# Kernel tuning notes

Hardware: AMD Instinct MI355X
Metric: run time of the kernel (lower is better)

Reference implementation:

```python
import jax, jax.numpy as jnp
import numpy as np

B = 524288       # number of parallel tracklets
S_DIM = 8        # state dim [x,y,z,vx,vy,vz,ax,ay]
O_DIM = 3        # observation dim [x,y,z]
DT = 0.1         # delta_t in seconds (10 Hz tracker step)


def build_F(dt: float) -> jnp.ndarray:
    """Constant-acceleration transition matrix, [8,8]."""
    dt2 = 0.5 * dt * dt
    F = np.eye(S_DIM, dtype=np.float32)
    F[0, 3] = dt; F[1, 4] = dt; F[2, 5] = dt
    F[0, 6] = dt2; F[1, 7] = dt2
    F[3, 6] = dt; F[4, 7] = dt
    return jnp.asarray(F)


def setup_inputs() -> dict:
    key = jax.random.key(0)
    kx, kP, kz = jax.random.split(key, 3)
    x = jax.random.normal(kx, (B, S_DIM, 1), dtype=jnp.float32)
    # PSD covariance: I + 0.1 * L @ L^T  (well-conditioned, non-trivial)
    L = 0.1 * jax.random.normal(kP, (B, S_DIM, S_DIM), dtype=jnp.float32)
    P = jnp.broadcast_to(jnp.eye(S_DIM, dtype=jnp.float32), (B, S_DIM, S_DIM)) \
        + jnp.matmul(L, jnp.swapaxes(L, -1, -2))
    z = jax.random.normal(kz, (B, O_DIM, 1), dtype=jnp.float32)
    # default process / measurement noise, as in the module's registered buffers
    Q = jnp.broadcast_to(0.01 * jnp.eye(S_DIM, dtype=jnp.float32), (B, S_DIM, S_DIM))
    R = jnp.broadcast_to(0.10 * jnp.eye(O_DIM, dtype=jnp.float32), (B, O_DIM, O_DIM))
    return {"x": x, "P": P, "z": z, "Q": Q, "R": R}


def reference(x, P, z, Q, R):
    """Batched EKF predict(DT, Q) followed by update(z, R).

    H = [I_3 | 0] selects the first 3 state components, so H @ A and A @ H^T
    are implemented as row/column slices (identical math, no materialized H).
    """
    F = build_F(DT)  # [8,8]
    # --- predict ---
    x_pred = jnp.einsum('ij,bjk->bik', F, x)             # [B,8,1]
    P_pred = jnp.einsum('ij,bjk,lk->bil', F, P, F) + Q   # F P F^T + Q, [B,8,8]
    # --- update ---
    S = P_pred[:, :O_DIM, :O_DIM] + R                    # H P H^T + R, [B,3,3]
    K = jnp.matmul(P_pred[:, :, :O_DIM], jnp.linalg.inv(S))  # P H^T S^{-1}, [B,8,3]
    innov = z - x_pred[:, :O_DIM, :]                     # z - H x, [B,3,1]
    x_upd = x_pred + jnp.matmul(K, innov)                # [B,8,1]
    # (I - K H) P = P - K (H P) = P - K @ P_pred[:, :3, :]
    P_upd = P_pred - jnp.matmul(K, P_pred[:, :O_DIM, :])  # [B,8,8]
    return x_upd, P_upd
```

## Files before the change

kernel.cpp:

```cpp
#include <hip/hip_runtime.h>


#define DT_C  0.1f
#define DT2_C 0.005f

__global__ __launch_bounds__(256) void ekf_kernel(
    const float* __restrict__ x_in,
    const float* __restrict__ P_in,
    const float* __restrict__ z_in,
    const float* __restrict__ Q_in,
    const float* __restrict__ R_in,
    float* __restrict__ out_x,
    float* __restrict__ out_P,
    int B)
{
    int b = blockIdx.x * blockDim.x + threadIdx.x;
    if (b >= B) return;

    float x[8];
    {
        const float4* p = reinterpret_cast<const float4*>(x_in + (size_t)b * 8);
        float4 a0 = p[0], a1 = p[1];
        x[0]=a0.x; x[1]=a0.y; x[2]=a0.z; x[3]=a0.w;
        x[4]=a1.x; x[5]=a1.y; x[6]=a1.z; x[7]=a1.w;
    }

    float P[64];
    {
        const float4* p = reinterpret_cast<const float4*>(P_in + (size_t)b * 64);
        #pragma unroll
        for (int i = 0; i < 16; ++i) {
            float4 v = p[i];
            P[4*i+0]=v.x; P[4*i+1]=v.y; P[4*i+2]=v.z; P[4*i+3]=v.w;
        }
    }

    float xp[8];
    xp[0] = x[0] + DT_C*x[3] + DT2_C*x[6];
    xp[1] = x[1] + DT_C*x[4] + DT2_C*x[7];
    xp[2] = x[2] + DT_C*x[5];
    xp[3] = x[3] + DT_C*x[6];
    xp[4] = x[4] + DT_C*x[7];
    xp[5] = x[5];
    xp[6] = x[6];
    xp[7] = x[7];

    #pragma unroll
    for (int j = 0; j < 8; ++j) {
        P[0*8+j] += DT_C*P[3*8+j] + DT2_C*P[6*8+j];
        P[1*8+j] += DT_C*P[4*8+j] + DT2_C*P[7*8+j];
        P[2*8+j] += DT_C*P[5*8+j];
        P[3*8+j] += DT_C*P[6*8+j];
        P[4*8+j] += DT_C*P[7*8+j];
    }
    #pragma unroll
    for (int i = 0; i < 8; ++i) {
        P[i*8+0] += DT_C*P[i*8+3] + DT2_C*P[i*8+6];
        P[i*8+1] += DT_C*P[i*8+4] + DT2_C*P[i*8+7];
        P[i*8+2] += DT_C*P[i*8+5];
        P[i*8+3] += DT_C*P[i*8+6];
        P[i*8+4] += DT_C*P[i*8+7];
    }
    {
        const float4* p = reinterpret_cast<const float4*>(Q_in + (size_t)b * 64);
        #pragma unroll
        for (int i = 0; i < 16; ++i) {
            float4 v = p[i];
            P[4*i+0]+=v.x; P[4*i+1]+=v.y; P[4*i+2]+=v.z; P[4*i+3]+=v.w;
        }
    }

    const float* Rb = R_in + (size_t)b * 9;
    float sa = P[0]  + Rb[0], sb = P[1]  + Rb[1], sc = P[2]  + Rb[2];
    float sd = P[8]  + Rb[3], se = P[9]  + Rb[4], sf = P[10] + Rb[5];
    float sg = P[16] + Rb[6], sh = P[17] + Rb[7], si = P[18] + Rb[8];

    float A0 = se*si - sf*sh;
    float A1 = sf*sg - sd*si;
    float A2 = sd*sh - se*sg;
    float det = sa*A0 + sb*A1 + sc*A2;
    float idet = 1.0f / det;
    float i00 = A0*idet;
    float i01 = (sc*sh - sb*si)*idet;
    float i02 = (sb*sf - sc*se)*idet;
    float i10 = A1*idet;
    float i11 = (sa*si - sc*sg)*idet;
    float i12 = (sc*sd - sa*sf)*idet;
    float i20 = A2*idet;
    float i21 = (sb*sg - sa*sh)*idet;
    float i22 = (sa*se - sb*sd)*idet;

    float K0[8], K1[8], K2[8];
    #pragma unroll
    for (int i = 0; i < 8; ++i) {
        float p0 = P[i*8+0], p1 = P[i*8+1], p2 = P[i*8+2];
        K0[i] = p0*i00 + p1*i10 + p2*i20;
        K1[i] = p0*i01 + p1*i11 + p2*i21;
        K2[i] = p0*i02 + p1*i12 + p2*i22;
    }

    const float* zb = z_in + (size_t)b * 3;
    float v0 = zb[0] - xp[0];
    float v1 = zb[1] - xp[1];
    float v2 = zb[2] - xp[2];

    {
        float xu[8];
        #pragma unroll
        for (int i = 0; i < 8; ++i)
            xu[i] = xp[i] + K0[i]*v0 + K1[i]*v1 + K2[i]*v2;
        float4* oxp = reinterpret_cast<float4*>(out_x + (size_t)b * 8);
        oxp[0] = make_float4(xu[0],xu[1],xu[2],xu[3]);
        oxp[1] = make_float4(xu[4],xu[5],xu[6],xu[7]);
    }

    float T0[8], T1[8], T2[8];
    #pragma unroll
    for (int j = 0; j < 8; ++j) { T0[j]=P[j]; T1[j]=P[8+j]; T2[j]=P[16+j]; }

    float4* oPp = reinterpret_cast<float4*>(out_P + (size_t)b * 64);
    #pragma unroll
    for (int i = 0; i < 8; ++i) {
        float r[8];
        #pragma unroll
        for (int j = 0; j < 8; ++j)
            r[j] = P[i*8+j] - (K0[i]*T0[j] + K1[i]*T1[j] + K2[i]*T2[j]);
        oPp[2*i+0] = make_float4(r[0],r[1],r[2],r[3]);
        oPp[2*i+1] = make_float4(r[4],r[5],r[6],r[7]);
    }
}

extern "C" void kernel_launch(void* const* d_in, const int* in_sizes, int n_in,
                              void* d_out, int out_size, void* d_ws, size_t ws_size,
                              hipStream_t stream) {
    const float* x = (const float*)d_in[0];
    const float* P = (const float*)d_in[1];
    const float* z = (const float*)d_in[2];
    const float* Q = (const float*)d_in[3];
    const float* R = (const float*)d_in[4];
    int B = in_sizes[0] / 8;

    float* out   = (float*)d_out;
    float* out_x = out;
    float* out_P = out + (size_t)B * 8;

    int block = 256;
    int grid = (B + block - 1) / block;
    ekf_kernel<<<grid, block, 0, stream>>>(x, P, z, Q, R, out_x, out_P, B);
}
```

Measured before the change: 399.5 us.

## Stage P, Q and R through LDS for coalesced global loads and stores

Each 64-thread block cooperatively loads its P, Q and R tiles from global memory with consecutive threads reading consecutive float4s. The tiles go into padded LDS, and each thread then reads its own matrix from there. Results are written back to LDS and stored out coalesced. A separate tail kernel handles leftover elements. This targets the strided per-thread 256-byte access pattern, at the cost of LDS usage, two barriers and reduced occupancy from the large shared allocation.

```diff
diff --git a/kernel.cpp b/kernel.cpp
--- a/kernel.cpp
+++ b/kernel.cpp
@@ -4,47 +4,10 @@
 #define DT_C  0.1f
 #define DT2_C 0.005f
 
-__global__ __launch_bounds__(256) void ekf_kernel(
-    const float* __restrict__ x_in,
-    const float* __restrict__ P_in,
-    const float* __restrict__ z_in,
-    const float* __restrict__ Q_in,
-    const float* __restrict__ R_in,
-    float* __restrict__ out_x,
-    float* __restrict__ out_P,
-    int B)
-{
-    int b = blockIdx.x * blockDim.x + threadIdx.x;
-    if (b >= B) return;
-
-    float x[8];
-    {
-        const float4* p = reinterpret_cast<const float4*>(x_in + (size_t)b * 8);
-        float4 a0 = p[0], a1 = p[1];
-        x[0]=a0.x; x[1]=a0.y; x[2]=a0.z; x[3]=a0.w;
-        x[4]=a1.x; x[5]=a1.y; x[6]=a1.z; x[7]=a1.w;
-    }
-
-    float P[64];
-    {
-        const float4* p = reinterpret_cast<const float4*>(P_in + (size_t)b * 64);
-        #pragma unroll
-        for (int i = 0; i < 16; ++i) {
-            float4 v = p[i];
-            P[4*i+0]=v.x; P[4*i+1]=v.y; P[4*i+2]=v.z; P[4*i+3]=v.w;
-        }
-    }
-
-    float xp[8];
-    xp[0] = x[0] + DT_C*x[3] + DT2_C*x[6];
-    xp[1] = x[1] + DT_C*x[4] + DT2_C*x[7];
-    xp[2] = x[2] + DT_C*x[5];
-    xp[3] = x[3] + DT_C*x[6];
-    xp[4] = x[4] + DT_C*x[7];
-    xp[5] = x[5];
-    xp[6] = x[6];
-    xp[7] = x[7];
-
+#define TPB   64
+#define ROWV4 17
+
+__device__ __forceinline__ void ekf_predict_rows_cols(float* P) {
     #pragma unroll
     for (int j = 0; j < 8; ++j) {
         P[0*8+j] += DT_C*P[3*8+j] + DT2_C*P[6*8+j];
@@ -61,19 +24,14 @@
         P[i*8+3] += DT_C*P[i*8+6];
         P[i*8+4] += DT_C*P[i*8+7];
     }
-    {
-        const float4* p = reinterpret_cast<const float4*>(Q_in + (size_t)b * 64);
-        #pragma unroll
-        for (int i = 0; i < 16; ++i) {
-            float4 v = p[i];
-            P[4*i+0]+=v.x; P[4*i+1]+=v.y; P[4*i+2]+=v.z; P[4*i+3]+=v.w;
-        }
-    }
-
-    const float* Rb = R_in + (size_t)b * 9;
-    float sa = P[0]  + Rb[0], sb = P[1]  + Rb[1], sc = P[2]  + Rb[2];
-    float sd = P[8]  + Rb[3], se = P[9]  + Rb[4], sf = P[10] + Rb[5];
-    float sg = P[16] + Rb[6], sh = P[17] + Rb[7], si = P[18] + Rb[8];
+}
+
+__device__ __forceinline__ void ekf_update(float* P, const float* xp,
+                                           float z0, float z1, float z2,
+                                           const float* Rl, float* xu) {
+    float sa = P[0]  + Rl[0], sb = P[1]  + Rl[1], sc = P[2]  + Rl[2];
+    float sd = P[8]  + Rl[3], se = P[9]  + Rl[4], sf = P[10] + Rl[5];
+    float sg = P[16] + Rl[6], sh = P[17] + Rl[7], si = P[18] + Rl[8];
 
     float A0 = se*si - sf*sh;
     float A1 = sf*sg - sd*si;
@@ -99,35 +57,187 @@
         K2[i] = p0*i02 + p1*i12 + p2*i22;
     }
 
-    const float* zb = z_in + (size_t)b * 3;
-    float v0 = zb[0] - xp[0];
-    float v1 = zb[1] - xp[1];
-    float v2 = zb[2] - xp[2];
-
-    {
-        float xu[8];
+    float v0 = z0 - xp[0];
+    float v1 = z1 - xp[1];
+    float v2 = z2 - xp[2];
+
+    #pragma unroll
+    for (int i = 0; i < 8; ++i)
+        xu[i] = xp[i] + K0[i]*v0 + K1[i]*v1 + K2[i]*v2;
+
+    float T0[8], T1[8], T2[8];
+    #pragma unroll
+    for (int j = 0; j < 8; ++j) { T0[j]=P[j]; T1[j]=P[8+j]; T2[j]=P[16+j]; }
+    #pragma unroll
+    for (int i = 0; i < 8; ++i) {
         #pragma unroll
-        for (int i = 0; i < 8; ++i)
-            xu[i] = xp[i] + K0[i]*v0 + K1[i]*v1 + K2[i]*v2;
-        float4* oxp = reinterpret_cast<float4*>(out_x + (size_t)b * 8);
+        for (int j = 0; j < 8; ++j)
+            P[i*8+j] -= K0[i]*T0[j] + K1[i]*T1[j] + K2[i]*T2[j];
+    }
+}
+
+__global__ __launch_bounds__(TPB) void ekf_kernel(
+    const float* __restrict__ x_in,
+    const float* __restrict__ P_in,
+    const float* __restrict__ z_in,
+    const float* __restrict__ Q_in,
+    const float* __restrict__ R_in,
+    float* __restrict__ out_x,
+    float* __restrict__ out_P)
+{
+    __shared__ float4 ldsP[TPB * ROWV4];
+    __shared__ float4 ldsQ[TPB * ROWV4];
+    __shared__ float  ldsR[TPB * 9];
+
+    const int t = threadIdx.x;
+    const long long blockBase = (long long)blockIdx.x * TPB;
+    const long long b = blockBase + t;
+
+    const float4* Pg = reinterpret_cast<const float4*>(P_in) + blockBase * 16;
+    const float4* Qg = reinterpret_cast<const float4*>(Q_in) + blockBase * 16;
+    const float*  Rg = R_in + blockBase * 9;
+
+    #pragma unroll
+    for (int k = 0; k < 16; ++k) {
+        int i = k * TPB + t;
+        int e = i >> 4, c = i & 15;
+        ldsP[e * ROWV4 + c] = Pg[i];
+        ldsQ[e * ROWV4 + c] = Qg[i];
+    }
+    #pragma unroll
+    for (int k = 0; k < 9; ++k) {
+        int i = k * TPB + t;
+        ldsR[i] = Rg[i];
+    }
+
+    float x[8];
+    {
+        const float4* p = reinterpret_cast<const float4*>(x_in + b * 8);
+        float4 a0 = p[0], a1 = p[1];
+        x[0]=a0.x; x[1]=a0.y; x[2]=a0.z; x[3]=a0.w;
+        x[4]=a1.x; x[5]=a1.y; x[6]=a1.z; x[7]=a1.w;
+    }
+    const float* zb = z_in + b * 3;
+    float z0 = zb[0], z1 = zb[1], z2 = zb[2];
+
+    __syncthreads();
+
+    float P[64];
+    #pragma unroll
+    for (int j = 0; j < 16; ++j) {
+        float4 v = ldsP[t * ROWV4 + j];
+        P[4*j+0]=v.x; P[4*j+1]=v.y; P[4*j+2]=v.z; P[4*j+3]=v.w;
+    }
+
+    float xp[8];
+    xp[0] = x[0] + DT_C*x[3] + DT2_C*x[6];
+    xp[1] = x[1] + DT_C*x[4] + DT2_C*x[7];
+    xp[2] = x[2] + DT_C*x[5];
+    xp[3] = x[3] + DT_C*x[6];
+    xp[4] = x[4] + DT_C*x[7];
+    xp[5] = x[5];
+    xp[6] = x[6];
+    xp[7] = x[7];
+
+    ekf_predict_rows_cols(P);
+
+    #pragma unroll
+    for (int j = 0; j < 16; ++j) {
+        float4 v = ldsQ[t * ROWV4 + j];
+        P[4*j+0]+=v.x; P[4*j+1]+=v.y; P[4*j+2]+=v.z; P[4*j+3]+=v.w;
+    }
+
+    float Rl[9];
+    #pragma unroll
+    for (int j = 0; j < 9; ++j) Rl[j] = ldsR[t * 9 + j];
+
+    float xu[8];
+    ekf_update(P, xp, z0, z1, z2, Rl, xu);
+
+    {
+        float4* oxp = reinterpret_cast<float4*>(out_x + b * 8);
         oxp[0] = make_float4(xu[0],xu[1],xu[2],xu[3]);
         oxp[1] = make_float4(xu[4],xu[5],xu[6],xu[7]);
     }
 
-    float T0[8], T1[8], T2[8];
-    #pragma unroll
-    for (int j = 0; j < 8; ++j) { T0[j]=P[j]; T1[j]=P[8+j]; T2[j]=P[16+j]; }
+    #pragma unroll
+    for (int j = 0; j < 16; ++j)
+        ldsP[t * ROWV4 + j] = make_float4(P[4*j+0],P[4*j+1],P[4*j+2],P[4*j+3]);
+
+    __syncthreads();
+
+    float4* Pog = reinterpret_cast<float4*>(out_P) + blockBase * 16;
+    #pragma unroll
+    for (int k = 0; k < 16; ++k) {
+        int i = k * TPB + t;
+        Pog[i] = ldsP[(i >> 4) * ROWV4 + (i & 15)];
+    }
+}
+
+__global__ __launch_bounds__(TPB) void ekf_tail_kernel(
+    const float* __restrict__ x_in,
+    const float* __restrict__ P_in,
+    const float* __restrict__ z_in,
+    const float* __restrict__ Q_in,
+    const float* __restrict__ R_in,
+    float* __restrict__ out_x,
+    float* __restrict__ out_P,
+    int first, int B)
+{
+    int b = first + (int)threadIdx.x;
+    if (b >= B) return;
+
+    float x[8];
+    {
+        const float4* p = reinterpret_cast<const float4*>(x_in + (size_t)b * 8);
+        float4 a0 = p[0], a1 = p[1];
+        x[0]=a0.x; x[1]=a0.y; x[2]=a0.z; x[3]=a0.w;
+        x[4]=a1.x; x[5]=a1.y; x[6]=a1.z; x[7]=a1.w;
+    }
+    float P[64];
+    {
+        const float4* p = reinterpret_cast<const float4*>(P_in + (size_t)b * 64);
+        #pragma unroll
+        for (int i = 0; i < 16; ++i) {
+            float4 v = p[i];
+            P[4*i+0]=v.x; P[4*i+1]=v.y; P[4*i+2]=v.z; P[4*i+3]=v.w;
+        }
+    }
+    float xp[8];
+    xp[0] = x[0] + DT_C*x[3] + DT2_C*x[6];
+    xp[1] = x[1] + DT_C*x[4] + DT2_C*x[7];
+    xp[2] = x[2] + DT_C*x[5];
+    xp[3] = x[3] + DT_C*x[6];
+    xp[4] = x[4] + DT_C*x[7];
+    xp[5] = x[5]; xp[6] = x[6]; xp[7] = x[7];
+
+    ekf_predict_rows_cols(P);
+
+    {
+        const float4* p = reinterpret_cast<const float4*>(Q_in + (size_t)b * 64);
+        #pragma unroll
+        for (int i = 0; i < 16; ++i) {
+            float4 v = p[i];
+            P[4*i+0]+=v.x; P[4*i+1]+=v.y; P[4*i+2]+=v.z; P[4*i+3]+=v.w;
+        }
+    }
+    const float* Rb = R_in + (size_t)b * 9;
+    float Rl[9];
+    #pragma unroll
+    for (int j = 0; j < 9; ++j) Rl[j] = Rb[j];
+    const float* zb = z_in + (size_t)b * 3;
+
+    float xu[8];
+    ekf_update(P, xp, zb[0], zb[1], zb[2], Rl, xu);
+
+    float4* oxp = reinterpret_cast<float4*>(out_x + (size_t)b * 8);
+    oxp[0] = make_float4(xu[0],xu[1],xu[2],xu[3]);
+    oxp[1] = make_float4(xu[4],xu[5],xu[6],xu[7]);
 
     float4* oPp = reinterpret_cast<float4*>(out_P + (size_t)b * 64);
     #pragma unroll
-    for (int i = 0; i < 8; ++i) {
-        float r[8];
-        #pragma unroll
-        for (int j = 0; j < 8; ++j)
-            r[j] = P[i*8+j] - (K0[i]*T0[j] + K1[i]*T1[j] + K2[i]*T2[j]);
-        oPp[2*i+0] = make_float4(r[0],r[1],r[2],r[3]);
-        oPp[2*i+1] = make_float4(r[4],r[5],r[6],r[7]);
-    }
+    for (int i = 0; i < 16; ++i)
+        oPp[i] = make_float4(P[4*i+0],P[4*i+1],P[4*i+2],P[4*i+3]);
 }
 
 extern "C" void kernel_launch(void* const* d_in, const int* in_sizes, int n_in,
@@ -144,7 +254,11 @@
     float* out_x = out;
     float* out_P = out + (size_t)B * 8;
 
-    int block = 256;
-    int grid = (B + block - 1) / block;
-    ekf_kernel<<<grid, block, 0, stream>>>(x, P, z, Q, R, out_x, out_P, B);
-}
+    int fullBlocks = B / TPB;
+    int rem = B % TPB;
+    if (fullBlocks > 0)
+        ekf_kernel<<<fullBlocks, TPB, 0, stream>>>(x, P, z, Q, R, out_x, out_P);
+    if (rem > 0)
+        ekf_tail_kernel<<<1, TPB, 0, stream>>>(x, P, z, Q, R, out_x, out_P,
+                                               fullBlocks * TPB, B);
+}
```

Measured after the change: 356.6 us. -10.7%, faster.

## Split each tracklet across 8 lanes, one covariance row per lane, using shuffles

Applied to the files above, without the earlier changes.

Instead of one thread holding the full 8x8 covariance, eight lanes each hold one row and exchange data through width-8 shuffles for the row update of F P F^T, the S matrix, and the K H P correction. Neighbouring lanes now read adjacent rows, so loads and stores coalesce better, and register pressure drops enough that a min-blocks-per-SM launch bound is added. The price is extra shuffle instructions and a 3x3 inverse that every lane of the group computes redundantly.

```diff
diff --git a/kernel.cpp b/kernel.cpp
--- a/kernel.cpp
+++ b/kernel.cpp
@@ -4,7 +4,7 @@
 #define DT_C  0.1f
 #define DT2_C 0.005f
 
-__global__ __launch_bounds__(256) void ekf_kernel(
+__global__ __launch_bounds__(256, 4) void ekf_kernel(
     const float* __restrict__ x_in,
     const float* __restrict__ P_in,
     const float* __restrict__ z_in,
@@ -14,66 +14,56 @@
     float* __restrict__ out_P,
     int B)
 {
-    int b = blockIdx.x * blockDim.x + threadIdx.x;
-    if (b >= B) return;
+    const long long tid = (long long)blockIdx.x * blockDim.x + threadIdx.x;
+    const long long e = tid >> 3;
+    const int r = (int)(tid & 7);
+    if (e >= B) return;
 
-    float x[8];
+    float p[8];
     {
-        const float4* p = reinterpret_cast<const float4*>(x_in + (size_t)b * 8);
-        float4 a0 = p[0], a1 = p[1];
-        x[0]=a0.x; x[1]=a0.y; x[2]=a0.z; x[3]=a0.w;
-        x[4]=a1.x; x[5]=a1.y; x[6]=a1.z; x[7]=a1.w;
+        const float4* Pg = reinterpret_cast<const float4*>(P_in + e * 64 + r * 8);
+        float4 a = Pg[0], b = Pg[1];
+        p[0]=a.x; p[1]=a.y; p[2]=a.z; p[3]=a.w;
+        p[4]=b.x; p[5]=b.y; p[6]=b.z; p[7]=b.w;
+    }
+    float xr = x_in[e * 8 + r];
+
+    const float coefA = (r <= 4) ? DT_C  : 0.0f;
+    const float coefB = (r <= 1) ? DT2_C : 0.0f;
+    const int srcA = (r + 3) & 7;
+    const int srcB = (r + 6) & 7;
+
+    float pn[8];
+    #pragma unroll
+    for (int j = 0; j < 8; ++j) {
+        float vA = __shfl(p[j], srcA, 8);
+        float vB = __shfl(p[j], srcB, 8);
+        pn[j] = p[j] + coefA * vA + coefB * vB;
     }
 
-    float P[64];
+    float xp = xr + coefA * __shfl(xr, srcA, 8) + coefB * __shfl(xr, srcB, 8);
+
+    pn[0] += DT_C*pn[3] + DT2_C*pn[6];
+    pn[1] += DT_C*pn[4] + DT2_C*pn[7];
+    pn[2] += DT_C*pn[5];
+    pn[3] += DT_C*pn[6];
+    pn[4] += DT_C*pn[7];
+
     {
-        const float4* p = reinterpret_cast<const float4*>(P_in + (size_t)b * 64);
-        #pragma unroll
-        for (int i = 0; i < 16; ++i) {
-            float4 v = p[i];
-            P[4*i+0]=v.x; P[4*i+1]=v.y; P[4*i+2]=v.z; P[4*i+3]=v.w;
-        }
+        const float4* Qg = reinterpret_cast<const float4*>(Q_in + e * 64 + r * 8);
+        float4 a = Qg[0], b = Qg[1];
+        pn[0]+=a.x; pn[1]+=a.y; pn[2]+=a.z; pn[3]+=a.w;
+        pn[4]+=b.x; pn[5]+=b.y; pn[6]+=b.z; pn[7]+=b.w;
     }
 
-    float xp[8];
-    xp[0] = x[0] + DT_C*x[3] + DT2_C*x[6];
-    xp[1] = x[1] + DT_C*x[4] + DT2_C*x[7];
-    xp[2] = x[2] + DT_C*x[5];
-    xp[3] = x[3] + DT_C*x[6];
-    xp[4] = x[4] + DT_C*x[7];
-    xp[5] = x[5];
-    xp[6] = x[6];
-    xp[7] = x[7];
+    float t00 = __shfl(pn[0], 0, 8), t01 = __shfl(pn[1], 0, 8), t02 = __shfl(pn[2], 0, 8);
+    float t10 = __shfl(pn[0], 1, 8), t11 = __shfl(pn[1], 1, 8), t12 = __shfl(pn[2], 1, 8);
+    float t20 = __shfl(pn[0], 2, 8), t21 = __shfl(pn[1], 2, 8), t22 = __shfl(pn[2], 2, 8);
 
-    #pragma unroll
-    for (int j = 0; j < 8; ++j) {
-        P[0*8+j] += DT_C*P[3*8+j] + DT2_C*P[6*8+j];
-        P[1*8+j] += DT_C*P[4*8+j] + DT2_C*P[7*8+j];
-        P[2*8+j] += DT_C*P[5*8+j];
-        P[3*8+j] += DT_C*P[6*8+j];
-        P[4*8+j] += DT_C*P[7*8+j];
-    }
-    #pragma unroll
-    for (int i = 0; i < 8; ++i) {
-        P[i*8+0] += DT_C*P[i*8+3] + DT2_C*P[i*8+6];
-        P[i*8+1] += DT_C*P[i*8+4] + DT2_C*P[i*8+7];
-        P[i*8+2] += DT_C*P[i*8+5];
-        P[i*8+3] += DT_C*P[i*8+6];
-        P[i*8+4] += DT_C*P[i*8+7];
-    }
-    {
-        const float4* p = reinterpret_cast<const float4*>(Q_in + (size_t)b * 64);
-        #pragma unroll
-        for (int i = 0; i < 16; ++i) {
-            float4 v = p[i];
-            P[4*i+0]+=v.x; P[4*i+1]+=v.y; P[4*i+2]+=v.z; P[4*i+3]+=v.w;
-        }
-    }
-
-    const float* Rb = R_in + (size_t)b * 9;
-    float sa = P[0]  + Rb[0], sb = P[1]  + Rb[1], sc = P[2]  + Rb[2];
-    float sd = P[8]  + Rb[3], se = P[9]  + Rb[4], sf = P[10] + Rb[5];
-    float sg = P[16] + Rb[6], sh = P[17] + Rb[7], si = P[18] + Rb[8];
+    const float* Rb = R_in + e * 9;
+    float sa = t00 + Rb[0], sb = t01 + Rb[1], sc = t02 + Rb[2];
+    float sd = t10 + Rb[3], se = t11 + Rb[4], sf = t12 + Rb[5];
+    float sg = t20 + Rb[6], sh = t21 + Rb[7], si = t22 + Rb[8];
 
     float A0 = se*si - sf*sh;
     float A1 = sf*sg - sd*si;
@@ -90,44 +80,33 @@
     float i21 = (sb*sg - sa*sh)*idet;
     float i22 = (sa*se - sb*sd)*idet;
 
-    float K0[8], K1[8], K2[8];
+    float K0 = pn[0]*i00 + pn[1]*i10 + pn[2]*i20;
+    float K1 = pn[0]*i01 + pn[1]*i11 + pn[2]*i21;
+    float K2 = pn[0]*i02 + pn[1]*i12 + pn[2]*i22;
+
+    float zr = z_in[e * 3 + (r < 3 ? r : 0)];
+    float dv = zr - xp;
+    float v0 = __shfl(dv, 0, 8);
+    float v1 = __shfl(dv, 1, 8);
+    float v2 = __shfl(dv, 2, 8);
+
+    out_x[e * 8 + r] = xp + K0*v0 + K1*v1 + K2*v2;
+
+    float res[8];
+    res[0] = pn[0] - (K0*t00 + K1*t10 + K2*t20);
+    res[1] = pn[1] - (K0*t01 + K1*t11 + K2*t21);
+    res[2] = pn[2] - (K0*t02 + K1*t12 + K2*t22);
     #pragma unroll
-    for (int i = 0; i < 8; ++i) {
-        float p0 = P[i*8+0], p1 = P[i*8+1], p2 = P[i*8+2];
-        K0[i] = p0*i00 + p1*i10 + p2*i20;
-        K1[i] = p0*i01 + p1*i11 + p2*i21;
-        K2[i] = p0*i02 + p1*i12 + p2*i22;
+    for (int j = 3; j < 8; ++j) {
+        float T0 = __shfl(pn[j], 0, 8);
+        float T1 = __shfl(pn[j], 1, 8);
+        float T2 = __shfl(pn[j], 2, 8);
+        res[j] = pn[j] - (K0*T0 + K1*T1 + K2*T2);
     }
 
-    const float* zb = z_in + (size_t)b * 3;
-    float v0 = zb[0] - xp[0];
-    float v1 = zb[1] - xp[1];
-    float v2 = zb[2] - xp[2];
-
-    {
-        float xu[8];
-        #pragma unroll
-        for (int i = 0; i < 8; ++i)
-            xu[i] = xp[i] + K0[i]*v0 + K1[i]*v1 + K2[i]*v2;
-        float4* oxp = reinterpret_cast<float4*>(out_x + (size_t)b * 8);
-        oxp[0] = make_float4(xu[0],xu[1],xu[2],xu[3]);
-        oxp[1] = make_float4(xu[4],xu[5],xu[6],xu[7]);
-    }
-
-    float T0[8], T1[8], T2[8];
-    #pragma unroll
-    for (int j = 0; j < 8; ++j) { T0[j]=P[j]; T1[j]=P[8+j]; T2[j]=P[16+j]; }
-
-    float4* oPp = reinterpret_cast<float4*>(out_P + (size_t)b * 64);
-    #pragma unroll
-    for (int i = 0; i < 8; ++i) {
-        float r[8];
-        #pragma unroll
-        for (int j = 0; j < 8; ++j)
-            r[j] = P[i*8+j] - (K0[i]*T0[j] + K1[i]*T1[j] + K2[i]*T2[j]);
-        oPp[2*i+0] = make_float4(r[0],r[1],r[2],r[3]);
-        oPp[2*i+1] = make_float4(r[4],r[5],r[6],r[7]);
-    }
+    float4* Pog = reinterpret_cast<float4*>(out_P + e * 64 + r * 8);
+    Pog[0] = make_float4(res[0], res[1], res[2], res[3]);
+    Pog[1] = make_float4(res[4], res[5], res[6], res[7]);
 }
 
 extern "C" void kernel_launch(void* const* d_in, const int* in_sizes, int n_in,
@@ -144,7 +123,8 @@
     float* out_x = out;
     float* out_P = out + (size_t)B * 8;
 
+    long long totalThreads = (long long)B * 8;
     int block = 256;
-    int grid = (B + block - 1) / block;
-    ekf_kernel<<<grid, block, 0, stream>>>(x, P, z, Q, R, out_x, out_P, B);
+    long long grid = (totalThreads + block - 1) / block;
+    ekf_kernel<<<(int)grid, block, 0, stream>>>(x, P, z, Q, R, out_x, out_P, B);
 }
```

After: 350.4 us. 1.14x faster.
